# Kernel tuning notes

Measured on AMD Instinct MI355X. Metric: run time of the kernel, lower is better.

Reference implementation:

```python
import jax, jax.numpy as jnp
import numpy as np

B, M, N, I, O, NM = 16, 256, 256, 64, 64, 16


def setup_inputs() -> dict:
    key = jax.random.key(0)
    k1, k2, k3, k4, k5 = jax.random.split(key, 5)
    glorot = 1.0 / np.sqrt(I + O)
    return {
        "x": jax.random.normal(k1, (B, M, N, I), dtype=jnp.float32),
        "fw1": jax.random.normal(k2, (I, O, NM, NM, 2), dtype=jnp.float32) * glorot,
        "fw2": jax.random.normal(k3, (I, O, NM, NM, 2), dtype=jnp.float32) * glorot,
        "W": jax.random.normal(k4, (I, O), dtype=jnp.float32) * glorot,
        "b": jnp.zeros((O,), dtype=jnp.float32),
    }


def reference(x, fw1, fw2, W, b):
    # x: [B, M, N, I] -> [B, I, M, N]
    Bs, Ms, Ns, Is = x.shape
    nm = fw1.shape[2]
    xt = jnp.transpose(x, (0, 3, 1, 2))
    # forward rFFT over spatial dims, scaled by 1/sqrt(M*N) as in the TF code
    x_ft = jnp.fft.rfft2(xt, s=(Ms, Ns))  # [B, I, M, N//2+1] complex64
    x_ft = x_ft / jnp.asarray(np.sqrt(Ms * Ns), dtype=x_ft.dtype)
    # complex weights (stack-of-2 real/imag -> complex); complex einsum is
    # exactly the real/imag stacked matmul in the original
    w1 = jax.lax.complex(fw1[..., 0], fw1[..., 1])
    w2 = jax.lax.complex(fw2[..., 0], fw2[..., 1])
    top = jnp.einsum('bixy,ioxy->boxy', x_ft[:, :, :nm, :nm], w1)
    bot = jnp.einsum('bixy,ioxy->boxy', x_ft[:, :, -nm:, :nm], w2)
    mid = jnp.zeros((Bs, top.shape[1], Ms - 2 * nm, nm), dtype=top.dtype)
    out_ft = jnp.concatenate([top, mid, bot], axis=2)          # [B, O, M, nm]
    pad = jnp.zeros((Bs, top.shape[1], Ms, Ms // 2 + 1 - nm), dtype=top.dtype)
    out_ft = jnp.concatenate([out_ft, pad], axis=3)            # [B, O, M, M//2+1]
    y = jnp.fft.irfft2(out_ft, s=(Ns, Ms))                     # [B, O, N, M]
    # TF rescale: sqrt(prod of last two dims of out_ft) = sqrt(N*(M//2+1))
    y = y * jnp.asarray(np.sqrt(Ns * (Ms // 2 + 1)), dtype=y.dtype)
    y = jnp.transpose(y, (0, 2, 3, 1))                         # [B, M, N, O]
    return jax.nn.relu(y @ W + b + y)
```

## Files before the change

kernel.cpp:

```cpp
#include <hip/hip_runtime.h>
#include <hip/hip_bf16.h>


#define PI2F 6.283185307179586f

typedef __attribute__((ext_vector_type(8))) short short8v;
typedef __attribute__((ext_vector_type(4))) float f32x4;

static __device__ __forceinline__ float bf16_to_f(unsigned short h) {
  union { unsigned int u; float f; } v; v.u = ((unsigned int)h) << 16; return v.f;
}
static __device__ __forceinline__ unsigned short f_to_bf16(float f) {
  unsigned int u = __float_as_uint(f);
  u += 0x7fffu + ((u >> 16) & 1u);
  return (unsigned short)(u >> 16);
}
static __device__ __forceinline__ unsigned int pack_bf16(float lo, float hi) {
  return (unsigned int)f_to_bf16(lo) | ((unsigned int)f_to_bf16(hi) << 16);
}

__global__ __launch_bounds__(256) void k_tab(unsigned short* __restrict__ Eg,
                                             unsigned short* __restrict__ CSg,
                                             const float* __restrict__ Wg,
                                             unsigned short* __restrict__ Wtb) {
  int t = threadIdx.x;
#pragma unroll
  for (int ky = 0; ky < 16; ++ky) {
    int idx = (ky * t) & 255;
    float ss, cc;
    sincosf(PI2F * (float)idx * (1.0f / 256.0f), &ss, &cc);
    Eg[(2 * ky) * 256 + t]     = f_to_bf16(cc);
    Eg[(2 * ky + 1) * 256 + t] = f_to_bf16(-ss);
    CSg[t * 32 + 2 * ky]       = f_to_bf16(cc);
    CSg[t * 32 + 2 * ky + 1]   = f_to_bf16(ss);
  }
#pragma unroll
  for (int k = 0; k < 16; ++k) {
    int p = k * 256 + t;
    Wtb[(p & 63) * 64 + (p >> 6)] = f_to_bf16(Wg[p]);
  }
}

__global__ __launch_bounds__(256) void k_wt(const float* __restrict__ fw1,
                                            const float* __restrict__ fw2,
                                            float2* __restrict__ wT) {
  int a  = blockIdx.x >> 3;
  int ic = blockIdx.x & 7;
  const float* w = (a < 16) ? fw1 : fw2;
  int xx = a & 15;
#pragma unroll
  for (int k = 0; k < 2; ++k) {
    int p = k * 256 + (int)threadIdx.x;
    int i = ic * 8 + (p >> 6);
    int o = p & 63;
    const float4* s4 = reinterpret_cast<const float4*>(
        w + ((((size_t)i * 64 + o) * 16 + xx) * 16) * 2);
#pragma unroll
    for (int j = 0; j < 8; ++j) {
      float4 q = s4[j];
      wT[(((size_t)(2 * j) * 32 + a) * 64 + i) * 64 + o]     = make_float2(q.x, q.y);
      wT[(((size_t)(2 * j + 1) * 32 + a) * 64 + i) * 64 + o] = make_float2(q.z, q.w);
    }
  }
}

__global__ __launch_bounds__(256) void k1_mfma(const float* __restrict__ x,
                                               const unsigned short* __restrict__ Eg,
                                               unsigned int* __restrict__ Tb) {
  __shared__ unsigned short El[32 * 264];
  int bm = blockIdx.x;
  int b = bm >> 8, m = bm & 255;
  int tid = threadIdx.x;

  {
    const unsigned int* src = reinterpret_cast<const unsigned int*>(Eg);
    unsigned int* dst = reinterpret_cast<unsigned int*>(El);
#pragma unroll
    for (int t = 0; t < 16; ++t) {
      int idx = t * 256 + tid;
      dst[(idx >> 7) * 132 + (idx & 127)] = src[idx];
    }
  }
  __syncthreads();

  int lane = tid & 63, w = tid >> 6;
  int r16 = lane & 15, g4 = lane >> 4;
  const float* xp = x + (size_t)bm * 16384 + (w * 16 + r16);

  f32x4 z = {0.f, 0.f, 0.f, 0.f};
  f32x4 acc0 = z, acc1 = z;

#pragma unroll
  for (int ks = 0; ks < 8; ++ks) {
    int nb = ks * 32 + g4 * 8;
    float xv[8];
#pragma unroll
    for (int j = 0; j < 8; ++j) xv[j] = xp[(size_t)(nb + j) * 64];
    short8v bfr;
#pragma unroll
    for (int j = 0; j < 8; ++j) bfr[j] = (short)f_to_bf16(xv[j]);
    short8v a0 = *reinterpret_cast<const short8v*>(&El[r16 * 264 + nb]);
    short8v a1 = *reinterpret_cast<const short8v*>(&El[(16 + r16) * 264 + nb]);
    acc0 = __builtin_amdgcn_mfma_f32_16x16x32_bf16(a0, bfr, acc0, 0, 0, 0);
    acc1 = __builtin_amdgcn_mfma_f32_16x16x32_bf16(a1, bfr, acc1, 0, 0, 0);
  }

  const float SC = 1.0f / 256.0f;
  int i = w * 16 + r16;
#pragma unroll
  for (int mt = 0; mt < 2; ++mt) {
    f32x4 av = (mt == 0) ? acc0 : acc1;
    int ky_a = mt * 8 + g4 * 2;
    Tb[((size_t)(b * 16 + ky_a) * 256 + m) * 64 + i]       = pack_bf16(av[0] * SC, av[1] * SC);
    Tb[((size_t)(b * 16 + ky_a + 1) * 256 + m) * 64 + i]   = pack_bf16(av[2] * SC, av[3] * SC);
  }
}

__global__ __launch_bounds__(256) void k2_fwd_m(const unsigned int* __restrict__ Tb,
                                                float* __restrict__ Xp) {
  int bx = blockIdx.x;
  int bky = bx & 255, mc = bx >> 8;
  int m0 = mc * 64;
  int ih = threadIdx.x & 15;
  int ag = threadIdx.x >> 4;
  const uint4* Tp4 = reinterpret_cast<const uint4*>(Tb) + (size_t)bky * 4096 + ih;

  float cd1, sd1n, cd2, sd2n;
  { float ss, cc; sincosf(PI2F * (float)ag * (1.0f / 256.0f), &ss, &cc); cd1 = cc; sd1n = -ss; }
  { float ss, cc; sincosf(PI2F * (float)(ag - 16) * (1.0f / 256.0f), &ss, &cc); cd2 = cc; sd2n = -ss; }
  float c1, s1, c2, s2;
  { int t = (ag * m0) & 255; float ss, cc; sincosf(PI2F * (float)t * (1.0f / 256.0f), &ss, &cc); c1 = cc; s1 = -ss; }
  { int t = ((ag + 240) * m0) & 255; float ss, cc; sincosf(PI2F * (float)t * (1.0f / 256.0f), &ss, &cc); c2 = cc; s2 = -ss; }

  float xr1[4], xi1[4], xr2[4], xi2[4];
#pragma unroll
  for (int ii = 0; ii < 4; ++ii) { xr1[ii] = xi1[ii] = xr2[ii] = xi2[ii] = 0.0f; }

#pragma unroll 4
  for (int m = 0; m < 64; ++m) {
    uint4 q = Tp4[(size_t)(m0 + m) * 16];
    unsigned int dv[4] = {q.x, q.y, q.z, q.w};
    float tre[4], tim[4];
#pragma unroll
    for (int ii = 0; ii < 4; ++ii) {
      tre[ii] = __uint_as_float(dv[ii] << 16);
      tim[ii] = __uint_as_float(dv[ii] & 0xffff0000u);
    }
#pragma unroll
    for (int ii = 0; ii < 4; ++ii) {
      xr1[ii] += tre[ii] * c1 - tim[ii] * s1;
      xi1[ii] += tre[ii] * s1 + tim[ii] * c1;
      xr2[ii] += tre[ii] * c2 - tim[ii] * s2;
      xi2[ii] += tre[ii] * s2 + tim[ii] * c2;
    }
    float cn;
    cn = c1 * cd1 - s1 * sd1n; s1 = c1 * sd1n + s1 * cd1; c1 = cn;
    cn = c2 * cd2 - s2 * sd2n; s2 = c2 * sd2n + s2 * cd2; c2 = cn;
  }

  float* Xb = Xp + (size_t)mc * 1048576;
  float* Xp1 = Xb + ((size_t)bky * 32 + ag) * 128 + ih * 8;
  float* Xp2 = Xb + ((size_t)bky * 32 + ag + 16) * 128 + ih * 8;
  reinterpret_cast<float4*>(Xp1)[0] = make_float4(xr1[0], xi1[0], xr1[1], xi1[1]);
  reinterpret_cast<float4*>(Xp1)[1] = make_float4(xr1[2], xi1[2], xr1[3], xi1[3]);
  reinterpret_cast<float4*>(Xp2)[0] = make_float4(xr2[0], xi2[0], xr2[1], xi2[1]);
  reinterpret_cast<float4*>(Xp2)[1] = make_float4(xr2[2], xi2[2], xr2[3], xi2[3]);
}

__global__ __launch_bounds__(256) void k3_mix(const float* __restrict__ Xp,
                                              const float* __restrict__ wT,
                                              float* __restrict__ OF) {
  int blk = blockIdx.x;
  int kyy = blk >> 5, a = blk & 31;
  __shared__ float wre[64 * 65];
  __shared__ float wim[64 * 65];
  __shared__ float xsh[16 * 128];

  const float2* wsrc = reinterpret_cast<const float2*>(wT) + (size_t)(kyy * 32 + a) * 4096;
#pragma unroll
  for (int k = 0; k < 16; ++k) {
    int p = k * 256 + (int)threadIdx.x;
    float2 v = wsrc[p];
    int i = p >> 6, o = p & 63;
    wre[i * 65 + o] = v.x;
    wim[i * 65 + o] = v.y;
  }
  {
    int bb = threadIdx.x >> 4, icn = threadIdx.x & 15;
    size_t off = ((size_t)(bb * 16 + kyy) * 32 + a) * 128;
    float4 a0 = make_float4(0.f, 0.f, 0.f, 0.f), a1 = a0;
#pragma unroll
    for (int c = 0; c < 4; ++c) {
      const float4* xsrc = reinterpret_cast<const float4*>(Xp + (size_t)c * 1048576 + off);
      float4 q0 = xsrc[icn * 2], q1 = xsrc[icn * 2 + 1];
      a0.x += q0.x; a0.y += q0.y; a0.z += q0.z; a0.w += q0.w;
      a1.x += q1.x; a1.y += q1.y; a1.z += q1.z; a1.w += q1.w;
    }
    float4* xdst = reinterpret_cast<float4*>(xsh + bb * 128);
    xdst[icn * 2]     = a0;
    xdst[icn * 2 + 1] = a1;
  }
  __syncthreads();

  int o = threadIdx.x & 63, bg = threadIdx.x >> 6;
#pragma unroll
  for (int bb = 0; bb < 4; ++bb) {
    int b = bg * 4 + bb;
    float ore = 0.0f, oim = 0.0f;
    for (int i = 0; i < 64; ++i) {
      float xr = xsh[b * 128 + 2 * i], xi = xsh[b * 128 + 2 * i + 1];
      float wr = wre[i * 65 + o],     wi = wim[i * 65 + o];
      ore += xr * wr - xi * wi;
      oim += xr * wi + xi * wr;
    }
    reinterpret_cast<float2*>(OF)[(((size_t)b * 16 + kyy) * 32 + a) * 64 + o] =
        make_float2(ore, oim);
  }
}

__global__ __launch_bounds__(256) void k4_inv_kx(const float* __restrict__ OF,
                                                 uint4* __restrict__ Gb4) {
  int bx = blockIdx.x;
  int b = bx >> 6, ug = (bx >> 2) & 15, chunk = bx & 3;
  __shared__ float ofs[16384];
  __shared__ float ct[256], st[256];
  {
    float ssv, ccv;
    sincosf(PI2F * (float)threadIdx.x * (1.0f / 256.0f), &ssv, &ccv);
    ct[threadIdx.x] = ccv;
    st[threadIdx.x] = ssv;
  }
  {
    const float4* src = reinterpret_cast<const float4*>(
        OF + ((size_t)b * 16 + chunk * 4) * 4096);
    float4* dst = reinterpret_cast<float4*>(ofs);
#pragma unroll
    for (int k = 0; k < 16; ++k) dst[k * 256 + threadIdx.x] = src[k * 256 + threadIdx.x];
  }
  __syncthreads();

  int o = threadIdx.x & 63, us = threadIdx.x >> 6;
  int u0 = ug * 16 + us * 4;
  const float SC2 = 0.002772904280510622f;

  float accr[4][4], acci[4][4];
#pragma unroll
  for (int du = 0; du < 4; ++du)
#pragma unroll
    for (int kyl = 0; kyl < 4; ++kyl) { accr[du][kyl] = 0.0f; acci[du][kyl] = 0.0f; }

  for (int a = 0; a < 32; ++a) {
    int kx = (a < 16) ? a : (224 + a);
    float ofr[4], ofi[4];
#pragma unroll
    for (int kyl = 0; kyl < 4; ++kyl) {
      ofr[kyl] = ofs[((kyl * 32 + a) * 64 + o) * 2];
      ofi[kyl] = ofs[((kyl * 32 + a) * 64 + o) * 2 + 1];
    }
#pragma unroll
    for (int du = 0; du < 4; ++du) {
      int t = (kx * (u0 + du)) & 255;
      float cv = ct[t], sv = st[t];
#pragma unroll
      for (int kyl = 0; kyl < 4; ++kyl) {
        accr[du][kyl] += ofr[kyl] * cv - ofi[kyl] * sv;
        acci[du][kyl] += ofr[kyl] * sv + ofi[kyl] * cv;
      }
    }
  }
#pragma unroll
  for (int du = 0; du < 4; ++du) {
    int u = u0 + du;
    unsigned int wv[4];
#pragma unroll
    for (int kyl = 0; kyl < 4; ++kyl) {
      int ky = chunk * 4 + kyl;
      float sc = SC2 * ((ky == 0) ? 1.0f : 2.0f);
      wv[kyl] = pack_bf16(accr[du][kyl] * sc, -acci[du][kyl] * sc);
    }
    uint4 pk; pk.x = wv[0]; pk.y = wv[1]; pk.z = wv[2]; pk.w = wv[3];
    Gb4[(((size_t)b * 256 + u) * 64 + o) * 4 + chunk] = pk;
  }
}

__global__ __launch_bounds__(256) void k5_mfma(const unsigned short* __restrict__ Gb,
                                               const unsigned short* __restrict__ CSg,
                                               const unsigned short* __restrict__ Wtb,
                                               const float* __restrict__ bias,
                                               float* __restrict__ out) {
  __shared__ unsigned short yl[256 * 72];

  int blk = blockIdx.x;
  int tid = threadIdx.x;
  int lane = tid & 63, w = tid >> 6;
  int r16 = lane & 15, g4 = lane >> 4;
  int kc0 = g4 * 8;

  f32x4 z = {0.f, 0.f, 0.f, 0.f};
  f32x4 acc[4][4];

  short8v af[4], bfx[4];
#pragma unroll
  for (int vt = 0; vt < 4; ++vt)
    af[vt] = *reinterpret_cast<const short8v*>(&CSg[(w * 64 + vt * 16 + r16) * 32 + kc0]);
#pragma unroll
  for (int ot = 0; ot < 4; ++ot)
    bfx[ot] = *reinterpret_cast<const short8v*>(
        &Gb[((size_t)blk * 64 + ot * 16 + r16) * 32 + kc0]);
#pragma unroll
  for (int vt = 0; vt < 4; ++vt)
#pragma unroll
    for (int ot = 0; ot < 4; ++ot)
      acc[vt][ot] = __builtin_amdgcn_mfma_f32_16x16x32_bf16(af[vt], bfx[ot], z, 0, 0, 0);

#pragma unroll
  for (int vt = 0; vt < 4; ++vt)
#pragma unroll
    for (int ot = 0; ot < 4; ++ot)
#pragma unroll
      for (int r = 0; r < 4; ++r)
        yl[(w * 64 + vt * 16 + g4 * 4 + r) * 72 + ot * 16 + r16] = f_to_bf16(acc[vt][ot][r]);
  __syncthreads();

#pragma unroll
  for (int ot = 0; ot < 4; ++ot) {
    float bv = bias[ot * 16 + r16];
#pragma unroll
    for (int vt = 0; vt < 4; ++vt)
#pragma unroll
      for (int r = 0; r < 4; ++r) acc[vt][ot][r] += bv;
  }

#pragma unroll
  for (int ks = 0; ks < 2; ++ks) {
    int k0 = ks * 32 + kc0;
    short8v ya[4], wb[4];
#pragma unroll
    for (int vt = 0; vt < 4; ++vt)
      ya[vt] = *reinterpret_cast<const short8v*>(&yl[(w * 64 + vt * 16 + r16) * 72 + k0]);
#pragma unroll
    for (int ot = 0; ot < 4; ++ot)
      wb[ot] = *reinterpret_cast<const short8v*>(&Wtb[(ot * 16 + r16) * 64 + k0]);
#pragma unroll
    for (int vt = 0; vt < 4; ++vt)
#pragma unroll
      for (int ot = 0; ot < 4; ++ot)
        acc[vt][ot] = __builtin_amdgcn_mfma_f32_16x16x32_bf16(ya[vt], wb[ot], acc[vt][ot], 0, 0, 0);
  }

  float* ob = out + (size_t)blk * 16384;
#pragma unroll
  for (int vt = 0; vt < 4; ++vt)
#pragma unroll
    for (int r = 0; r < 4; ++r) {
      int v = w * 64 + vt * 16 + g4 * 4 + r;
      float* op = ob + (size_t)v * 64 + r16;
#pragma unroll
      for (int ot = 0; ot < 4; ++ot)
        op[ot * 16] = fmaxf(acc[vt][ot][r], 0.0f);
    }
}

extern "C" void kernel_launch(void* const* d_in, const int* in_sizes, int n_in,
                              void* d_out, int out_size, void* d_ws, size_t ws_size,
                              hipStream_t stream) {
  const float* x   = (const float*)d_in[0];
  const float* fw1 = (const float*)d_in[1];
  const float* fw2 = (const float*)d_in[2];
  const float* W   = (const float*)d_in[3];
  const float* bb  = (const float*)d_in[4];
  float* out = (float*)d_out;

  float* ws = (float*)d_ws;
  float* wT          = ws;
  unsigned int* Tb   = (unsigned int*)(ws + 4194304);
  float* Xp          = ws + 8388608;
  float* OF          = ws + 12582912;
  unsigned int* Gb   = (unsigned int*)(ws + 13631488);
  unsigned short* Eg  = (unsigned short*)(ws + 17825792);
  unsigned short* CSg = Eg + 8192;
  unsigned short* Wtb = CSg + 8192;

  hipLaunchKernelGGL(k_tab,    dim3(1),    dim3(256), 0, stream, Eg, CSg, W, Wtb);
  hipLaunchKernelGGL(k_wt,     dim3(256),  dim3(256), 0, stream, fw1, fw2, (float2*)wT);
  hipLaunchKernelGGL(k1_mfma,  dim3(4096), dim3(256), 0, stream, x, Eg, Tb);
  hipLaunchKernelGGL(k2_fwd_m, dim3(1024), dim3(256), 0, stream, Tb, Xp);
  hipLaunchKernelGGL(k3_mix,   dim3(512),  dim3(256), 0, stream, Xp, wT, OF);
  hipLaunchKernelGGL(k4_inv_kx,dim3(1024), dim3(256), 0, stream, OF, (uint4*)Gb);
  hipLaunchKernelGGL(k5_mfma,  dim3(4096), dim3(256), 0, stream,
                     (const unsigned short*)Gb, CSg, Wtb, bb, out);
}
```

Baseline: 241.2 us.

## Stage x and output through LDS for coalesced access and merge prep kernels

The table and weight-transpose prep kernels are merged into a single launch, with an extra block building the tables. In k1, each block's x row is loaded with coalesced float4 reads into a double-buffered LDS tile. This replaces strided per-lane global reads, at the cost of a __syncthreads each iteration. In k5, the __syncthreads after the yl write is removed (each wave only reads rows it wrote). The ReLU output is also transposed through per-wave LDS scratch so global stores are full float4 rows instead of scattered scalar writes.

```diff
diff --git a/kernel.cpp b/kernel.cpp
--- a/kernel.cpp
+++ b/kernel.cpp
@@ -7,9 +7,6 @@
 typedef __attribute__((ext_vector_type(8))) short short8v;
 typedef __attribute__((ext_vector_type(4))) float f32x4;
 
-static __device__ __forceinline__ float bf16_to_f(unsigned short h) {
-  union { unsigned int u; float f; } v; v.u = ((unsigned int)h) << 16; return v.f;
-}
 static __device__ __forceinline__ unsigned short f_to_bf16(float f) {
   unsigned int u = __float_as_uint(f);
   u += 0x7fffu + ((u >> 16) & 1u);
@@ -19,38 +16,39 @@
   return (unsigned int)f_to_bf16(lo) | ((unsigned int)f_to_bf16(hi) << 16);
 }
 
-__global__ __launch_bounds__(256) void k_tab(unsigned short* __restrict__ Eg,
-                                             unsigned short* __restrict__ CSg,
-                                             const float* __restrict__ Wg,
-                                             unsigned short* __restrict__ Wtb) {
+__global__ __launch_bounds__(256) void k_prep(const float* __restrict__ fw1,
+                                              const float* __restrict__ fw2,
+                                              float2* __restrict__ wT,
+                                              unsigned short* __restrict__ Eg,
+                                              unsigned short* __restrict__ CSg,
+                                              const float* __restrict__ Wg,
+                                              unsigned short* __restrict__ Wtb) {
   int t = threadIdx.x;
-#pragma unroll
-  for (int ky = 0; ky < 16; ++ky) {
-    int idx = (ky * t) & 255;
-    float ss, cc;
-    sincosf(PI2F * (float)idx * (1.0f / 256.0f), &ss, &cc);
-    Eg[(2 * ky) * 256 + t]     = f_to_bf16(cc);
-    Eg[(2 * ky + 1) * 256 + t] = f_to_bf16(-ss);
-    CSg[t * 32 + 2 * ky]       = f_to_bf16(cc);
-    CSg[t * 32 + 2 * ky + 1]   = f_to_bf16(ss);
-  }
-#pragma unroll
-  for (int k = 0; k < 16; ++k) {
-    int p = k * 256 + t;
-    Wtb[(p & 63) * 64 + (p >> 6)] = f_to_bf16(Wg[p]);
-  }
-}
-
-__global__ __launch_bounds__(256) void k_wt(const float* __restrict__ fw1,
-                                            const float* __restrict__ fw2,
-                                            float2* __restrict__ wT) {
+  if (blockIdx.x == 256) {
+#pragma unroll
+    for (int ky = 0; ky < 16; ++ky) {
+      int idx = (ky * t) & 255;
+      float ss, cc;
+      sincosf(PI2F * (float)idx * (1.0f / 256.0f), &ss, &cc);
+      Eg[(2 * ky) * 256 + t]     = f_to_bf16(cc);
+      Eg[(2 * ky + 1) * 256 + t] = f_to_bf16(-ss);
+      CSg[t * 32 + 2 * ky]       = f_to_bf16(cc);
+      CSg[t * 32 + 2 * ky + 1]   = f_to_bf16(ss);
+    }
+#pragma unroll
+    for (int k = 0; k < 16; ++k) {
+      int p = k * 256 + t;
+      Wtb[(p & 63) * 64 + (p >> 6)] = f_to_bf16(Wg[p]);
+    }
+    return;
+  }
   int a  = blockIdx.x >> 3;
   int ic = blockIdx.x & 7;
   const float* w = (a < 16) ? fw1 : fw2;
   int xx = a & 15;
 #pragma unroll
   for (int k = 0; k < 2; ++k) {
-    int p = k * 256 + (int)threadIdx.x;
+    int p = k * 256 + t;
     int i = ic * 8 + (p >> 6);
     int o = p & 63;
     const float4* s4 = reinterpret_cast<const float4*>(
@@ -67,7 +65,8 @@
 __global__ __launch_bounds__(256) void k1_mfma(const float* __restrict__ x,
                                                const unsigned short* __restrict__ Eg,
                                                unsigned int* __restrict__ Tb) {
-  __shared__ unsigned short El[32 * 264];
+  __shared__ __align__(16) unsigned short El[32 * 264];
+  __shared__ __align__(16) float xs[2][2048];
   int bm = blockIdx.x;
   int b = bm >> 8, m = bm & 255;
   int tid = threadIdx.x;
@@ -81,28 +80,46 @@
       dst[(idx >> 7) * 132 + (idx & 127)] = src[idx];
     }
   }
-  __syncthreads();
-
+
+  const float* xrow = x + (size_t)bm * 16384;
   int lane = tid & 63, w = tid >> 6;
   int r16 = lane & 15, g4 = lane >> 4;
-  const float* xp = x + (size_t)bm * 16384 + (w * 16 + r16);
+
+  {
+    const float4* s = reinterpret_cast<const float4*>(xrow);
+    float4 v0 = s[tid], v1 = s[256 + tid];
+    float4* d = reinterpret_cast<float4*>(xs[0]);
+    d[tid] = v0;
+    d[256 + tid] = v1;
+  }
+  __syncthreads();
 
   f32x4 z = {0.f, 0.f, 0.f, 0.f};
   f32x4 acc0 = z, acc1 = z;
 
 #pragma unroll
-  for (int ks = 0; ks < 8; ++ks) {
-    int nb = ks * 32 + g4 * 8;
+  for (int c = 0; c < 8; ++c) {
+    int cur = c & 1;
+    if (c < 7) {
+      const float4* s = reinterpret_cast<const float4*>(xrow + (c + 1) * 2048);
+      float4 v0 = s[tid], v1 = s[256 + tid];
+      float4* d = reinterpret_cast<float4*>(xs[cur ^ 1]);
+      d[tid] = v0;
+      d[256 + tid] = v1;
+    }
+    const float* xb = &xs[cur][g4 * 8 * 64 + (w * 16 + r16)];
     float xv[8];
 #pragma unroll
-    for (int j = 0; j < 8; ++j) xv[j] = xp[(size_t)(nb + j) * 64];
+    for (int j = 0; j < 8; ++j) xv[j] = xb[j * 64];
     short8v bfr;
 #pragma unroll
     for (int j = 0; j < 8; ++j) bfr[j] = (short)f_to_bf16(xv[j]);
+    int nb = c * 32 + g4 * 8;
     short8v a0 = *reinterpret_cast<const short8v*>(&El[r16 * 264 + nb]);
     short8v a1 = *reinterpret_cast<const short8v*>(&El[(16 + r16) * 264 + nb]);
     acc0 = __builtin_amdgcn_mfma_f32_16x16x32_bf16(a0, bfr, acc0, 0, 0, 0);
     acc1 = __builtin_amdgcn_mfma_f32_16x16x32_bf16(a1, bfr, acc1, 0, 0, 0);
+    __syncthreads();
   }
 
   const float SC = 1.0f / 256.0f;
@@ -111,8 +128,8 @@
   for (int mt = 0; mt < 2; ++mt) {
     f32x4 av = (mt == 0) ? acc0 : acc1;
     int ky_a = mt * 8 + g4 * 2;
-    Tb[((size_t)(b * 16 + ky_a) * 256 + m) * 64 + i]       = pack_bf16(av[0] * SC, av[1] * SC);
-    Tb[((size_t)(b * 16 + ky_a + 1) * 256 + m) * 64 + i]   = pack_bf16(av[2] * SC, av[3] * SC);
+    Tb[((size_t)(b * 16 + ky_a) * 256 + m) * 64 + i]     = pack_bf16(av[0] * SC, av[1] * SC);
+    Tb[((size_t)(b * 16 + ky_a + 1) * 256 + m) * 64 + i] = pack_bf16(av[2] * SC, av[3] * SC);
   }
 }
 
@@ -288,7 +305,7 @@
                                                const unsigned short* __restrict__ Wtb,
                                                const float* __restrict__ bias,
                                                float* __restrict__ out) {
-  __shared__ unsigned short yl[256 * 72];
+  __shared__ __align__(16) unsigned short yl[256 * 72];
 
   int blk = blockIdx.x;
   int tid = threadIdx.x;
@@ -320,7 +337,6 @@
 #pragma unroll
       for (int r = 0; r < 4; ++r)
         yl[(w * 64 + vt * 16 + g4 * 4 + r) * 72 + ot * 16 + r16] = f_to_bf16(acc[vt][ot][r]);
-  __syncthreads();
 
 #pragma unroll
   for (int ot = 0; ot < 4; ++ot) {
@@ -349,16 +365,22 @@
   }
 
   float* ob = out + (size_t)blk * 16384;
-#pragma unroll
-  for (int vt = 0; vt < 4; ++vt)
-#pragma unroll
-    for (int r = 0; r < 4; ++r) {
-      int v = w * 64 + vt * 16 + g4 * 4 + r;
-      float* op = ob + (size_t)v * 64 + r16;
-#pragma unroll
-      for (int ot = 0; ot < 4; ++ot)
-        op[ot * 16] = fmaxf(acc[vt][ot][r], 0.0f);
-    }
+  float* tw = reinterpret_cast<float*>(&yl[w * 4608]);
+#pragma unroll
+  for (int vt = 0; vt < 4; ++vt) {
+#pragma unroll
+    for (int ot = 0; ot < 4; ++ot)
+#pragma unroll
+      for (int r = 0; r < 4; ++r)
+        tw[(g4 * 4 + r) * 68 + ot * 16 + r16] = fmaxf(acc[vt][ot][r], 0.0f);
+    float* obase = ob + (size_t)(w * 64 + vt * 16) * 64;
+#pragma unroll
+    for (int q = 0; q < 4; ++q) {
+      float4 vv = *reinterpret_cast<const float4*>(
+          &tw[(q * 4 + (lane >> 4)) * 68 + (lane & 15) * 4]);
+      *reinterpret_cast<float4*>(&obase[q * 256 + lane * 4]) = vv;
+    }
+  }
 }
 
 extern "C" void kernel_launch(void* const* d_in, const int* in_sizes, int n_in,
@@ -381,8 +403,8 @@
   unsigned short* CSg = Eg + 8192;
   unsigned short* Wtb = CSg + 8192;
 
-  hipLaunchKernelGGL(k_tab,    dim3(1),    dim3(256), 0, stream, Eg, CSg, W, Wtb);
-  hipLaunchKernelGGL(k_wt,     dim3(256),  dim3(256), 0, stream, fw1, fw2, (float2*)wT);
+  hipLaunchKernelGGL(k_prep,   dim3(257),  dim3(256), 0, stream,
+                     fw1, fw2, (float2*)wT, Eg, CSg, W, Wtb);
   hipLaunchKernelGGL(k1_mfma,  dim3(4096), dim3(256), 0, stream, x, Eg, Tb);
   hipLaunchKernelGGL(k2_fwd_m, dim3(1024), dim3(256), 0, stream, Tb, Xp);
   hipLaunchKernelGGL(k3_mix,   dim3(512),  dim3(256), 0, stream, Xp, wT, OF);
```

After: 233.6 us. 1.03x faster.
